# Kernel tuning notes

Hardware: AMD Instinct MI355X
Metric: run time of the kernel (lower is better)

The kernel has to match this reference:

```python
import jax, jax.numpy as jnp
import numpy as np

NEG_SLOPE = 0.01  # torch F.leaky_relu default

def _leaky(v):
    return jnp.where(v > 0, v, NEG_SLOPE * v)

def _gcn_conv(h, W, b, row, col, n_nodes):
    # PyG GCNConv with add_self_loops=True, symmetric normalization:
    # out = D^{-1/2} (A + I) D^{-1/2} (h @ W) + b,  deg includes self loop (+1)
    xw = h @ W                                            # [N, H]
    deg = jnp.zeros((n_nodes,), xw.dtype).at[col].add(1.0) + 1.0
    dis = jax.lax.rsqrt(deg)
    norm = dis[row] * dis[col]                            # [E]
    agg = jnp.zeros_like(xw).at[col].add(norm[:, None] * xw[row])
    agg = agg + xw * (1.0 / deg)[:, None]                 # self-loop term: dis_i^2 = 1/deg_i
    return agg + b

def setup_inputs() -> dict:
    key = jax.random.key(0)
    ks = jax.random.split(key, 16)
    N, E, EL = 100000, 1600000, 200000
    IN, H, EA = 256, 64, 8
    s = 0.05
    return {
        "x": jax.random.normal(ks[0], (N, IN), jnp.float32),
        "edge_index": jax.random.randint(ks[1], (2, E), 0, N, jnp.int64),
        "edge_label_index": jax.random.randint(ks[2], (2, EL), 0, N, jnp.int64),
        "edge_attr": jax.random.normal(ks[3], (EL, EA), jnp.float32),
        "W1": jax.random.normal(ks[4], (IN, 128), jnp.float32) * s,
        "b1": jnp.zeros((128,), jnp.float32),
        "W2": jax.random.normal(ks[5], (128, H), jnp.float32) * s,
        "b2": jnp.zeros((H,), jnp.float32),
        "Wg1": jax.random.normal(ks[6], (H, H), jnp.float32) * s,
        "bg1": jnp.zeros((H,), jnp.float32),
        "Wg2": jax.random.normal(ks[7], (H, H), jnp.float32) * s,
        "bg2": jnp.zeros((H,), jnp.float32),
        "Wp": jax.random.normal(ks[8], (2 * H + EA, 1), jnp.float32) * s,
        "bp": jnp.zeros((1,), jnp.float32),
    }

def reference(x, edge_index, edge_label_index, edge_attr,
              W1, b1, W2, b2, Wg1, bg1, Wg2, bg2, Wp, bp):
    n_nodes = x.shape[0]
    row, col = edge_index[0], edge_index[1]
    # preprocess MLP (dropout p=0.0 -> identity)
    h = _leaky(x @ W1 + b1)
    h = _leaky(h @ W2 + b2)
    # two GCN layers
    h = _leaky(_gcn_conv(h, Wg1, bg1, row, col, n_nodes))
    h = _leaky(_gcn_conv(h, Wg2, bg2, row, col, n_nodes))
    # edge scoring head: gather-concat-linear
    h_src = h[edge_label_index[0]]
    h_dst = h[edge_label_index[1]]
    combined = jnp.concatenate([h_src, h_dst, edge_attr], axis=1)
    out = (combined @ Wp + bp).reshape(-1)
    return (out, h)
```

## Files before the change

kernel.cpp:

```cpp
#include <hip/hip_runtime.h>
#include <hip/hip_bf16.h>

typedef __attribute__((ext_vector_type(8))) short bf16x8;
typedef __attribute__((ext_vector_type(4))) float f32x4;

#define BSHIFT 8
#define BW 256
#define NSTR 8
#define BCAP 768
#define LCAP 24
#define KEDGE 16

__device__ __forceinline__ float lk(float v) { return v > 0.f ? v : 0.01f * v; }

__device__ __forceinline__ short f2b(float v) {
  union { __hip_bfloat16 h; short s; } u;
  u.h = __float2bfloat16(v);
  return u.s;
}
__device__ __forceinline__ float loadF(const void* p, size_t i, int f32) {
  return f32 ? ((const float*)p)[i]
             : __bfloat162float(((const __hip_bfloat16*)p)[i]);
}
__device__ __forceinline__ void storeF(void* p, size_t i, int f32, float v) {
  if (f32) ((float*)p)[i] = v;
  else     ((__hip_bfloat16*)p)[i] = __float2bfloat16(v);
}
__device__ __forceinline__ int loadI(const int* p, size_t base, size_t e, int i64) {
  return i64 ? p[2 * (base + e)] : p[base + e];
}
__device__ __forceinline__ float blo(unsigned u) {
  union { unsigned u; float f; } c; c.u = u << 16; return c.f;
}
__device__ __forceinline__ float bhi(unsigned u) {
  union { unsigned u; float f; } c; c.u = u & 0xffff0000u; return c.f;
}

__global__ void detect_kernel(const unsigned short* __restrict__ x,
                              const int* __restrict__ ei, int* __restrict__ flags) {
  int t = threadIdx.x;
  unsigned short u = x[t];
  int ex = (u >> 7) & 0xFF;
  if (ex >= 0xC0) atomicOr(&flags[0], 1);
  if (t < 128 && ei[2 * t + 1] != 0) atomicOr(&flags[1], 1);
}

__global__ __launch_bounds__(64) void pack_w_kernel(const void* __restrict__ W,
                                                    __hip_bfloat16* __restrict__ P,
                                                    int N, const int* __restrict__ flags) {
  int f32 = flags[0] != 0;
  int ks = blockIdx.x, ct = blockIdx.y, KS = gridDim.x;
  int lane = threadIdx.x;
  int g = lane >> 4, m = lane & 15;
  size_t base = ((size_t)(ct * KS + ks) * 64 + (size_t)lane) * 8;
#pragma unroll
  for (int j = 0; j < 8; ++j)
    P[base + j] = __float2bfloat16(
        loadF(W, (size_t)(ks * 32 + g * 8 + j) * N + (size_t)(ct * 16 + m), f32));
}

template <int KS, int CT, int AMODE>
__global__ __launch_bounds__(256) void gemm_pipe(const void* __restrict__ A,
                                                 const __hip_bfloat16* __restrict__ Bp,
                                                 const void* __restrict__ bias,
                                                 void* __restrict__ Out, int out_bf16,
                                                 __hip_bfloat16* __restrict__ Yout,
                                                 const float* __restrict__ dinv,
                                                 int M, int N, int act,
                                                 const int* __restrict__ flags) {
  constexpr int K = KS * 32;
  constexpr int CPR = K / 8;
  constexpr int TILEB = 32 * K * 2;
  constexpr int PPR = K / 8;
  constexpr int PP = K / 64;
  __shared__ char lds[2 * TILEB];
  int f32 = AMODE ? (flags[0] != 0) : 0;
  int tid = threadIdx.x;
  int lane = tid & 63;
  int w = tid >> 6;
  int m = lane & 15, g = lane >> 4;
  int nt = (M + 31) >> 5;
  if ((int)blockIdx.x >= nt) return;

  float4 sr[2 * PP > 0 ? 2 * PP : 2];

  auto loadregs = [&](int t) {
    const float* Af = (const float*)A;
    int row0 = t << 5;
#pragma unroll
    for (int j = 0; j < PP; ++j) {
      int q = j * 256 + tid;
      int r = q / PPR;
      int pc = q - r * PPR;
      int gr = row0 + r; if (gr >= M) gr = M - 1;
      const float* src = Af + (size_t)gr * K + (size_t)pc * 8;
      sr[2 * j]     = *(const float4*)src;
      sr[2 * j + 1] = *(const float4*)(src + 4);
    }
  };
  auto cvtwrite = [&](char* buf) {
#pragma unroll
    for (int j = 0; j < PP; ++j) {
      int q = j * 256 + tid;
      int r = q / PPR;
      int pc = q - r * PPR;
      bf16x8 ov;
      ov[0] = f2b(sr[2 * j].x);     ov[1] = f2b(sr[2 * j].y);
      ov[2] = f2b(sr[2 * j].z);     ov[3] = f2b(sr[2 * j].w);
      ov[4] = f2b(sr[2 * j + 1].x); ov[5] = f2b(sr[2 * j + 1].y);
      ov[6] = f2b(sr[2 * j + 1].z); ov[7] = f2b(sr[2 * j + 1].w);
      *(bf16x8*)(buf + (size_t)r * (K * 2) + (size_t)((pc ^ (r & 7)) * 16)) = ov;
    }
  };
  auto gstage = [&](int t, char* buf) {
    int row0 = t << 5;
    constexpr int PERW = 32 * CPR / 4;
#pragma unroll
    for (int i = 0; i < PERW; i += 64) {
      int p = w * PERW + i + lane;
      int r = p / CPR;
      int pc = p - r * CPR;
      int gr = row0 + r; if (gr >= M) gr = M - 1;
      const char* src = (const char*)A + (size_t)gr * (K * 2) +
                        (size_t)((pc ^ (r & 7)) * 16);
      char* dst = buf + (size_t)(w * PERW + i) * 16;
      __builtin_amdgcn_global_load_lds(
          (const __attribute__((address_space(1))) void*)src,
          (__attribute__((address_space(3))) void*)dst, 16, 0, 0);
    }
  };

  const __hip_bfloat16* bbase = Bp + ((size_t)(w * CT) * KS * 64 + (size_t)lane) * 8;
  float bv[CT];
#pragma unroll
  for (int cc = 0; cc < CT; ++cc)
    bv[cc] = bias ? loadF(bias, (size_t)((w * CT + cc) * 16 + m), flags[0] != 0) : 0.f;

  int t0 = blockIdx.x;
  if (f32) { loadregs(t0); cvtwrite(lds); }
  else     { gstage(t0, lds); }
  __syncthreads();

  int cur = 0;
  for (int t = t0; t < nt; t += gridDim.x) {
    int tn = t + gridDim.x;
    int have = tn < nt;
    char* bufc = lds + cur * TILEB;
    char* bufn = lds + (cur ^ 1) * TILEB;
    if (have) { if (f32) loadregs(tn); else gstage(tn, bufn); }

    f32x4 accs[2][CT];
#pragma unroll
    for (int tt = 0; tt < 2; ++tt)
#pragma unroll
      for (int cc = 0; cc < CT; ++cc) accs[tt][cc] = (f32x4){0, 0, 0, 0};
#pragma unroll
    for (int ks = 0; ks < KS; ++ks) {
      bf16x8 a[2];
#pragma unroll
      for (int tt = 0; tt < 2; ++tt) {
        int r = tt * 16 + m;
        int c = ks * 4 + g;
        a[tt] = *(const bf16x8*)(bufc + (size_t)r * (K * 2) +
                                 (size_t)((c ^ (r & 7)) * 16));
      }
      const __hip_bfloat16* bb = bbase + (size_t)ks * 64 * 8;
#pragma unroll
      for (int cc = 0; cc < CT; ++cc) {
        bf16x8 b = *(const bf16x8*)(bb + (size_t)cc * KS * 64 * 8);
#pragma unroll
        for (int tt = 0; tt < 2; ++tt)
          accs[tt][cc] = __builtin_amdgcn_mfma_f32_16x16x32_bf16(a[tt], b, accs[tt][cc], 0, 0, 0);
      }
    }
    int row0 = t << 5;
#pragma unroll
    for (int tt = 0; tt < 2; ++tt) {
#pragma unroll
      for (int r = 0; r < 4; ++r) {
        int ro = row0 + tt * 16 + g * 4 + r;
        if (ro < M) {
          float di = Yout ? dinv[ro] : 0.f;
#pragma unroll
          for (int cc = 0; cc < CT; ++cc) {
            int col = (w * CT + cc) * 16 + m;
            float v = accs[tt][cc][r] + bv[cc];
            if (act) v = lk(v);
            if (Out) {
              if (out_bf16) ((__hip_bfloat16*)Out)[(size_t)ro * N + col] = __float2bfloat16(v);
              else          ((float*)Out)[(size_t)ro * N + col] = v;
            }
            if (Yout) Yout[(size_t)ro * N + col] = __float2bfloat16(v * di);
          }
        }
      }
    }
    if (have && f32) cvtwrite(bufn);
    __syncthreads();
    cur ^= 1;
  }
}

__global__ __launch_bounds__(256) void bin_kernel(const int* __restrict__ ei,
                                                  int* __restrict__ cur,
                                                  int2* __restrict__ rec,
                                                  int E, int NB,
                                                  const int* __restrict__ flags) {
  extern __shared__ int lds[];
  int* bcnt = lds;
  int* gbase = lds + NB;
  int2* bins = (int2*)(lds + 2 * NB);
  int i64 = flags[1] == 0;
  int stripe = __builtin_amdgcn_s_getreg(63508) & (NSTR - 1);
  int t = threadIdx.x;
  const int perRound = 256 * KEDGE;
  for (int base = blockIdx.x * perRound; base < E; base += gridDim.x * perRound) {
    for (int b = t; b < NB; b += 256) bcnt[b] = 0;
    __syncthreads();
#pragma unroll 1
    for (int k = 0; k < KEDGE; ++k) {
      int i = base + k * 256 + t;
      if (i < E) {
        int r, c;
        if (i64) {
          r = ((const int2*)ei)[i].x;
          c = ((const int2*)ei)[(size_t)E + i].x;
        } else {
          r = ei[i];
          c = ei[(size_t)E + i];
        }
        int b = c >> BSHIFT;
        int pos = atomicAdd(&bcnt[b], 1);
        if (pos < LCAP) {
          bins[b * LCAP + pos] = make_int2(r, c);
        } else {
          int bs = b * NSTR + stripe;
          int slot = atomicAdd(&cur[bs], 1);
          if (slot < BCAP) rec[(size_t)bs * BCAP + slot] = make_int2(r, c);
        }
      }
    }
    __syncthreads();
    for (int b = t; b < NB; b += 256) {
      int n = min(bcnt[b], LCAP);
      if (n > 0) gbase[b] = atomicAdd(&cur[b * NSTR + stripe], n);
    }
    __syncthreads();
    int lane = t & 63, w = t >> 6;
    for (int b = w; b < NB; b += 4) {
      int n = min(bcnt[b], LCAP);
      if (n == 0) continue;
      int gb = gbase[b];
      size_t sb = (size_t)(b * NSTR + stripe) * BCAP;
      if (lane < n && gb + lane < BCAP)
        rec[sb + gb + lane] = bins[b * LCAP + lane];
    }
    __syncthreads();
  }
}

__global__ __launch_bounds__(512) void bucket_scan(const int* __restrict__ cur,
                                                   int* __restrict__ bbase, int NB) {
  __shared__ int lds[512];
  int t = threadIdx.x;
  int tot = 0;
  if (t < NB)
#pragma unroll
    for (int s = 0; s < NSTR; ++s) tot += min(cur[t * NSTR + s], BCAP);
  lds[t] = tot; __syncthreads();
  for (int o = 1; o < 512; o <<= 1) {
    int a = (t >= o) ? lds[t - o] : 0; __syncthreads();
    lds[t] += a; __syncthreads();
  }
  if (t < NB) bbase[t] = lds[t] - tot;
}

__global__ __launch_bounds__(512) void place_kernel(const int2* __restrict__ rec,
                                                    const int* __restrict__ cur,
                                                    const int* __restrict__ bbase,
                                                    int* __restrict__ rowptr,
                                                    int* __restrict__ csr,
                                                    float* __restrict__ dinv, int Nn) {
  int b = blockIdx.x;
  int lo = b << BSHIFT;
  int t = threadIdx.x;
  __shared__ int cnt[BW];
  __shared__ int sc[BW];
  __shared__ int cursor[BW];
  if (t < BW) cnt[t] = 0;
  __syncthreads();
#pragma unroll 1
  for (int s = 0; s < NSTR; ++s) {
    int n = min(cur[b * NSTR + s], BCAP);
    const int2* rp = rec + (size_t)(b * NSTR + s) * BCAP;
    for (int j = t; j < n; j += 512) atomicAdd(&cnt[rp[j].y - lo], 1);
  }
  __syncthreads();
  int v = 0;
  if (t < BW) { v = cnt[t]; sc[t] = v; }
  __syncthreads();
  for (int o = 1; o < BW; o <<= 1) {
    int a = (t >= o && t < BW) ? sc[t - o] : 0;
    __syncthreads();
    if (t < BW) sc[t] += a;
    __syncthreads();
  }
  if (t < BW) {
    int base = bbase[b];
    int col = lo + t;
    if (col < Nn) {
      rowptr[col] = base + sc[t];
      dinv[col] = rsqrtf((float)v + 1.0f);
    }
    cursor[t] = base + sc[t] - v;
  }
  __syncthreads();
#pragma unroll 1
  for (int s = 0; s < NSTR; ++s) {
    int n = min(cur[b * NSTR + s], BCAP);
    const int2* rp = rec + (size_t)(b * NSTR + s) * BCAP;
    for (int j = t; j < n; j += 512) {
      int2 e = rp[j];
      int pos = atomicAdd(&cursor[e.y - lo], 1);
      csr[pos] = e.x;
    }
  }
}

__global__ __launch_bounds__(256) void gather_kernel(const __hip_bfloat16* __restrict__ y,
                                                     const int* __restrict__ csr,
                                                     const int* __restrict__ rowptr,
                                                     const float* __restrict__ dinv,
                                                     const void* __restrict__ bias,
                                                     void* __restrict__ outp, size_t obase,
                                                     int out_use_flag, int Nn,
                                                     float* __restrict__ ssrc,
                                                     float* __restrict__ sdst,
                                                     const void* __restrict__ Wp,
                                                     const int* __restrict__ flags) {
  int f32 = flags[0] != 0;
  int of32 = out_use_flag ? f32 : 0;
  int lane = threadIdx.x & 63;
  int w = (blockIdx.x * blockDim.x + threadIdx.x) >> 6;
  if (2 * w >= Nn) return;
  int half = lane >> 5;
  int hl = lane & 31;
  int hb = half << 5;
  int node = 2 * w + half;
  int alive = node < Nn;
  int nd = alive ? node : Nn - 1;
  int s = (nd == 0) ? 0 : rowptr[nd - 1];
  int e = rowptr[nd];
  if (!alive) e = s;
  const unsigned* yu = (const unsigned*)y;
  float p0a = 0, p1a = 0, p0b = 0, p1b = 0;
  float p0c = 0, p1c = 0, p0d = 0, p1d = 0;
  for (int base = s; base < e; base += 32) {
    int cnt = e - base; if (cnt > 32) cnt = 32;
    int rl = (base + hl < e) ? csr[base + hl] : 0;
    int j = 0;
    for (; j + 8 <= cnt; j += 8) {
      int r0 = __shfl(rl, hb + j + 0, 64);
      int r1 = __shfl(rl, hb + j + 1, 64);
      int r2 = __shfl(rl, hb + j + 2, 64);
      int r3 = __shfl(rl, hb + j + 3, 64);
      int r4 = __shfl(rl, hb + j + 4, 64);
      int r5 = __shfl(rl, hb + j + 5, 64);
      int r6 = __shfl(rl, hb + j + 6, 64);
      int r7 = __shfl(rl, hb + j + 7, 64);
      unsigned u0 = yu[(unsigned)r0 * 32u + hl];
      unsigned u1 = yu[(unsigned)r1 * 32u + hl];
      unsigned u2 = yu[(unsigned)r2 * 32u + hl];
      unsigned u3 = yu[(unsigned)r3 * 32u + hl];
      unsigned u4 = yu[(unsigned)r4 * 32u + hl];
      unsigned u5 = yu[(unsigned)r5 * 32u + hl];
      unsigned u6 = yu[(unsigned)r6 * 32u + hl];
      unsigned u7 = yu[(unsigned)r7 * 32u + hl];
      p0a += blo(u0); p1a += bhi(u0);
      p0b += blo(u1); p1b += bhi(u1);
      p0c += blo(u2); p1c += bhi(u2);
      p0d += blo(u3); p1d += bhi(u3);
      p0a += blo(u4); p1a += bhi(u4);
      p0b += blo(u5); p1b += bhi(u5);
      p0c += blo(u6); p1c += bhi(u6);
      p0d += blo(u7); p1d += bhi(u7);
    }
    for (; j + 4 <= cnt; j += 4) {
      int r0 = __shfl(rl, hb + j + 0, 64);
      int r1 = __shfl(rl, hb + j + 1, 64);
      int r2 = __shfl(rl, hb + j + 2, 64);
      int r3 = __shfl(rl, hb + j + 3, 64);
      unsigned u0 = yu[(unsigned)r0 * 32u + hl];
      unsigned u1 = yu[(unsigned)r1 * 32u + hl];
      unsigned u2 = yu[(unsigned)r2 * 32u + hl];
      unsigned u3 = yu[(unsigned)r3 * 32u + hl];
      p0a += blo(u0); p1a += bhi(u0);
      p0b += blo(u1); p1b += bhi(u1);
      p0c += blo(u2); p1c += bhi(u2);
      p0d += blo(u3); p1d += bhi(u3);
    }
    for (; j < cnt; ++j) {
      int r0 = __shfl(rl, hb + j, 64);
      unsigned u0 = yu[(unsigned)r0 * 32u + hl];
      p0a += blo(u0); p1a += bhi(u0);
    }
  }
  float acc0 = (p0a + p0b) + (p0c + p0d);
  float acc1 = (p1a + p1b) + (p1c + p1d);
  unsigned un = yu[(unsigned)nd * 32u + hl];
  acc0 += blo(un); acc1 += bhi(un);
  float di = dinv[nd];
  int f = hl * 2;
  float v0 = lk(di * acc0 + loadF(bias, (size_t)f, f32));
  float v1 = lk(di * acc1 + loadF(bias, (size_t)(f + 1), f32));
  if (alive) {
    if (of32) {
      *(float2*)((float*)outp + obase + (size_t)node * 64 + f) = make_float2(v0, v1);
    } else {
      union { unsigned u; unsigned short ss[2]; } pk;
      pk.ss[0] = (unsigned short)f2b(v0);
      pk.ss[1] = (unsigned short)f2b(v1);
      *(unsigned*)((__hip_bfloat16*)outp + obase + (size_t)node * 64 + f) = pk.u;
    }
  }
  if (ssrc) {
    float q1 = v0 * loadF(Wp, (size_t)f, f32) + v1 * loadF(Wp, (size_t)(f + 1), f32);
    float q2 = v0 * loadF(Wp, (size_t)(64 + f), f32) + v1 * loadF(Wp, (size_t)(65 + f), f32);
#pragma unroll
    for (int o = 16; o > 0; o >>= 1) {
      q1 += __shfl_down(q1, o, 64);
      q2 += __shfl_down(q2, o, 64);
    }
    if (hl == 0 && alive) { ssrc[node] = q1; sdst[node] = q2; }
  }
}

__global__ __launch_bounds__(256) void edge_head_kernel(void* __restrict__ dout,
                                                        const int* __restrict__ eli,
                                                        const void* __restrict__ ea,
                                                        const float* __restrict__ ssrc,
                                                        const float* __restrict__ sdst,
                                                        const void* __restrict__ Wp,
                                                        const void* __restrict__ bp,
                                                        int EL, const int* __restrict__ flags) {
  int f32 = flags[0] != 0;
  int i64 = flags[1] == 0;
  int tid = blockIdx.x * blockDim.x + threadIdx.x;
  if (tid >= EL) return;
  int s = loadI(eli, 0, (size_t)tid, i64);
  int d = loadI(eli, (size_t)EL, (size_t)tid, i64);
  float acc = ssrc[s] + sdst[d] + loadF(bp, 0, f32);
  if (f32) {
    const float* eap = (const float*)ea + (size_t)tid * 8;
    float4 u0 = *(const float4*)eap;
    float4 u1 = *(const float4*)(eap + 4);
    acc += u0.x * loadF(Wp, 128, 1) + u0.y * loadF(Wp, 129, 1) +
           u0.z * loadF(Wp, 130, 1) + u0.w * loadF(Wp, 131, 1) +
           u1.x * loadF(Wp, 132, 1) + u1.y * loadF(Wp, 133, 1) +
           u1.z * loadF(Wp, 134, 1) + u1.w * loadF(Wp, 135, 1);
  } else {
    bf16x8 u = *(const bf16x8*)((const __hip_bfloat16*)ea + (size_t)tid * 8);
#pragma unroll
    for (int j = 0; j < 8; ++j) {
      union { short s; __hip_bfloat16 h; } cv; cv.s = u[j];
      acc += __bfloat162float(cv.h) * loadF(Wp, (size_t)(128 + j), 0);
    }
  }
  storeF(dout, (size_t)tid, f32, acc);
}

extern "C" void kernel_launch(void* const* d_in, const int* in_sizes, int n_in,
                              void* d_out, int out_size, void* d_ws, size_t ws_size,
                              hipStream_t stream) {
  const void* x   = d_in[0];
  const int* ei   = (const int*)d_in[1];
  const int* eli  = (const int*)d_in[2];
  const void* ea  = d_in[3];
  const void* W1  = d_in[4];
  const void* b1  = d_in[5];
  const void* W2  = d_in[6];
  const void* b2  = d_in[7];
  const void* Wg1 = d_in[8];
  const void* bg1 = d_in[9];
  const void* Wg2 = d_in[10];
  const void* bg2 = d_in[11];
  const void* Wp  = d_in[12];
  const void* bp  = d_in[13];

  const int Nn = in_sizes[0] / 256;
  const int E  = in_sizes[1] / 2;
  const int EL = in_sizes[2] / 2;
  const int NB = (Nn + BW - 1) >> BSHIFT;

  char* ws = (char*)d_ws;
  size_t off = 0;
  auto take = [&](size_t bytes) -> char* {
    char* p = ws + off;
    off = (off + bytes + 255) & ~(size_t)255;
    return p;
  };
  int*   flags  = (int*)take(256);
  int*   cur    = (int*)take((size_t)NB * NSTR * 4);
  int*   bbase  = (int*)take((size_t)NB * 4);
  int*   rowptr = (int*)take((size_t)Nn * 4);
  float* dinv   = (float*)take((size_t)Nn * 4);
  float* ssrc   = (float*)take((size_t)Nn * 4);
  float* sdst   = (float*)take((size_t)Nn * 4);
  int*   csr    = (int*)take((size_t)E * 4);
  int2*  rec    = (int2*)take((size_t)NB * NSTR * BCAP * 8);
  __hip_bfloat16* pW1 = (__hip_bfloat16*)take(256 * 128 * 2);
  __hip_bfloat16* pW2 = (__hip_bfloat16*)take(128 * 64 * 2);
  __hip_bfloat16* pG1 = (__hip_bfloat16*)take(64 * 64 * 2);
  __hip_bfloat16* pG2 = (__hip_bfloat16*)take(64 * 64 * 2);
  char* regionA = take((size_t)Nn * 128 * 4);
  char* regionB = take((size_t)Nn * 64 * 4);
  __hip_bfloat16* h1 = (__hip_bfloat16*)regionA;
  __hip_bfloat16* y = (__hip_bfloat16*)(regionA + (size_t)Nn * 64 * 4);
  __hip_bfloat16* h2 = (__hip_bfloat16*)regionB;
  __hip_bfloat16* h3 = (__hip_bfloat16*)regionB;

  hipMemsetAsync(flags, 0, 256 + (((size_t)NB * NSTR * 4 + 255) & ~(size_t)255), stream);
  detect_kernel<<<1, 256, 0, stream>>>((const unsigned short*)x, ei, flags);

  dim3 b64(64);
  pack_w_kernel<<<dim3(8, 8), b64, 0, stream>>>(W1, pW1, 128, flags);
  pack_w_kernel<<<dim3(4, 4), b64, 0, stream>>>(W2, pW2, 64, flags);
  pack_w_kernel<<<dim3(2, 4), b64, 0, stream>>>(Wg1, pG1, 64, flags);
  pack_w_kernel<<<dim3(2, 4), b64, 0, stream>>>(Wg2, pG2, 64, flags);

  const int ldsbytes = NB * (8 + LCAP * 8);
  const int nbin = (E + 256 * KEDGE - 1) / (256 * KEDGE);
  bin_kernel<<<nbin, 256, ldsbytes, stream>>>(ei, cur, rec, E, NB, flags);
  bucket_scan<<<1, 512, 0, stream>>>(cur, bbase, NB);
  place_kernel<<<NB, 512, 0, stream>>>(rec, cur, bbase, rowptr, csr, dinv, Nn);

  const int nt = (Nn + 31) / 32;
  const int pgrid = nt < 1024 ? nt : 1024;
  gemm_pipe<8, 2, 1><<<pgrid, 256, 0, stream>>>(x, pW1, b1, h1, 1, nullptr, nullptr,
                                                Nn, 128, 1, flags);
  gemm_pipe<4, 1, 0><<<pgrid, 256, 0, stream>>>(h1, pW2, b2, h2, 1, nullptr, nullptr,
                                                Nn, 64, 1, flags);

  const int gwaves = (Nn + 1) / 2;
  const int gblocks = (gwaves + 3) / 4;
  gemm_pipe<2, 1, 0><<<pgrid, 256, 0, stream>>>(h2, pG1, nullptr, nullptr, 0, y, dinv,
                                                Nn, 64, 0, flags);
  gather_kernel<<<gblocks, 256, 0, stream>>>(y, csr, rowptr, dinv, bg1,
                                             h3, 0, 0, Nn,
                                             nullptr, nullptr, nullptr, flags);

  gemm_pipe<2, 1, 0><<<pgrid, 256, 0, stream>>>(h3, pG2, nullptr, nullptr, 0, y, dinv,
                                                Nn, 64, 0, flags);
  gather_kernel<<<gblocks, 256, 0, stream>>>(y, csr, rowptr, dinv, bg2,
                                             d_out, (size_t)EL, 1, Nn,
                                             ssrc, sdst, Wp, flags);

  edge_head_kernel<<<(EL + 255) / 256, 256, 0, stream>>>(d_out, eli, ea, ssrc, sdst,
                                                         Wp, bp, EL, flags);
}
```

Before: 402.6 us.

## Merge weight packing launches, fold bucket scan into place, use one-tile-per-block GEMMs

The four weight-pack launches are merged into one 96-block kernel, and the separate single-block bucket_scan is removed. Each place_kernel block now computes its own prefix base by reducing the counts of all preceding buckets. The persistent double-buffered GEMM is replaced by a simple one-tile-per-block kernel launched over all row tiles, trading prefetch overlap for more resident blocks and less loop bookkeeping. Together these cut kernel-launch count and serial dependencies, at the cost of redundant per-block prefix reductions and no explicit load/compute pipelining.

```diff
diff --git a/kernel.cpp b/kernel.cpp
--- a/kernel.cpp
+++ b/kernel.cpp
@@ -45,11 +45,22 @@
   if (t < 128 && ei[2 * t + 1] != 0) atomicOr(&flags[1], 1);
 }
 
-__global__ __launch_bounds__(64) void pack_w_kernel(const void* __restrict__ W,
-                                                    __hip_bfloat16* __restrict__ P,
-                                                    int N, const int* __restrict__ flags) {
+__global__ __launch_bounds__(64) void pack_all(const void* __restrict__ W1,
+                                               const void* __restrict__ W2,
+                                               const void* __restrict__ G1,
+                                               const void* __restrict__ G2,
+                                               __hip_bfloat16* __restrict__ P1,
+                                               __hip_bfloat16* __restrict__ P2,
+                                               __hip_bfloat16* __restrict__ PG1,
+                                               __hip_bfloat16* __restrict__ PG2,
+                                               const int* __restrict__ flags) {
   int f32 = flags[0] != 0;
-  int ks = blockIdx.x, ct = blockIdx.y, KS = gridDim.x;
+  int b = blockIdx.x;
+  const void* W; __hip_bfloat16* P; int KS, N, ks, ct;
+  if (b < 64)      { W = W1; P = P1;  KS = 8; N = 128; int c = b;      ks = c & 7; ct = c >> 3; }
+  else if (b < 80) { W = W2; P = P2;  KS = 4; N = 64;  int c = b - 64; ks = c & 3; ct = c >> 2; }
+  else if (b < 88) { W = G1; P = PG1; KS = 2; N = 64;  int c = b - 80; ks = c & 1; ct = c >> 1; }
+  else             { W = G2; P = PG2; KS = 2; N = 64;  int c = b - 88; ks = c & 1; ct = c >> 1; }
   int lane = threadIdx.x;
   int g = lane >> 4, m = lane & 15;
   size_t base = ((size_t)(ct * KS + ks) * 64 + (size_t)lane) * 8;
@@ -60,144 +71,120 @@
 }
 
 template <int KS, int CT, int AMODE>
-__global__ __launch_bounds__(256) void gemm_pipe(const void* __restrict__ A,
-                                                 const __hip_bfloat16* __restrict__ Bp,
-                                                 const void* __restrict__ bias,
-                                                 void* __restrict__ Out, int out_bf16,
-                                                 __hip_bfloat16* __restrict__ Yout,
-                                                 const float* __restrict__ dinv,
-                                                 int M, int N, int act,
-                                                 const int* __restrict__ flags) {
+__global__ __launch_bounds__(256) void gemm_bt(const void* __restrict__ A,
+                                               const __hip_bfloat16* __restrict__ Bp,
+                                               const void* __restrict__ bias,
+                                               void* __restrict__ Out, int out_bf16,
+                                               __hip_bfloat16* __restrict__ Yout,
+                                               const float* __restrict__ dinv,
+                                               int M, int N, int act,
+                                               const int* __restrict__ flags) {
   constexpr int K = KS * 32;
   constexpr int CPR = K / 8;
-  constexpr int TILEB = 32 * K * 2;
-  constexpr int PPR = K / 8;
-  constexpr int PP = K / 64;
-  __shared__ char lds[2 * TILEB];
+  __shared__ char tile[32 * K * 2];
   int f32 = AMODE ? (flags[0] != 0) : 0;
   int tid = threadIdx.x;
   int lane = tid & 63;
   int w = tid >> 6;
   int m = lane & 15, g = lane >> 4;
-  int nt = (M + 31) >> 5;
-  if ((int)blockIdx.x >= nt) return;
-
-  float4 sr[2 * PP > 0 ? 2 * PP : 2];
-
-  auto loadregs = [&](int t) {
-    const float* Af = (const float*)A;
-    int row0 = t << 5;
-#pragma unroll
-    for (int j = 0; j < PP; ++j) {
-      int q = j * 256 + tid;
-      int r = q / PPR;
-      int pc = q - r * PPR;
-      int gr = row0 + r; if (gr >= M) gr = M - 1;
-      const float* src = Af + (size_t)gr * K + (size_t)pc * 8;
-      sr[2 * j]     = *(const float4*)src;
-      sr[2 * j + 1] = *(const float4*)(src + 4);
-    }
-  };
-  auto cvtwrite = [&](char* buf) {
-#pragma unroll
-    for (int j = 0; j < PP; ++j) {
-      int q = j * 256 + tid;
-      int r = q / PPR;
-      int pc = q - r * PPR;
-      bf16x8 ov;
-      ov[0] = f2b(sr[2 * j].x);     ov[1] = f2b(sr[2 * j].y);
-      ov[2] = f2b(sr[2 * j].z);     ov[3] = f2b(sr[2 * j].w);
-      ov[4] = f2b(sr[2 * j + 1].x); ov[5] = f2b(sr[2 * j + 1].y);
-      ov[6] = f2b(sr[2 * j + 1].z); ov[7] = f2b(sr[2 * j + 1].w);
-      *(bf16x8*)(buf + (size_t)r * (K * 2) + (size_t)((pc ^ (r & 7)) * 16)) = ov;
-    }
-  };
-  auto gstage = [&](int t, char* buf) {
-    int row0 = t << 5;
+  int row0 = blockIdx.x << 5;
+
+  bool done = false;
+  if constexpr (AMODE) {
+    if (f32) {
+      constexpr int PP = K / 64;
+      float4 sr[2 * PP];
+#pragma unroll
+      for (int j = 0; j < PP; ++j) {
+        int q = j * 256 + tid;
+        int r = q / CPR, pc = q - r * CPR;
+        int gr = row0 + r; if (gr >= M) gr = M - 1;
+        const float* src = (const float*)A + (size_t)gr * K + (size_t)pc * 8;
+        sr[2 * j]     = *(const float4*)src;
+        sr[2 * j + 1] = *(const float4*)(src + 4);
+      }
+#pragma unroll
+      for (int j = 0; j < PP; ++j) {
+        int q = j * 256 + tid;
+        int r = q / CPR, pc = q - r * CPR;
+        bf16x8 ov;
+        ov[0] = f2b(sr[2 * j].x);     ov[1] = f2b(sr[2 * j].y);
+        ov[2] = f2b(sr[2 * j].z);     ov[3] = f2b(sr[2 * j].w);
+        ov[4] = f2b(sr[2 * j + 1].x); ov[5] = f2b(sr[2 * j + 1].y);
+        ov[6] = f2b(sr[2 * j + 1].z); ov[7] = f2b(sr[2 * j + 1].w);
+        *(bf16x8*)(tile + (size_t)r * (K * 2) + (size_t)((pc ^ (r & 7)) * 16)) = ov;
+      }
+      done = true;
+    }
+  }
+  if (!done) {
     constexpr int PERW = 32 * CPR / 4;
 #pragma unroll
     for (int i = 0; i < PERW; i += 64) {
       int p = w * PERW + i + lane;
-      int r = p / CPR;
-      int pc = p - r * CPR;
+      int r = p / CPR, pc = p - r * CPR;
       int gr = row0 + r; if (gr >= M) gr = M - 1;
       const char* src = (const char*)A + (size_t)gr * (K * 2) +
                         (size_t)((pc ^ (r & 7)) * 16);
-      char* dst = buf + (size_t)(w * PERW + i) * 16;
+      char* dst = tile + (size_t)(w * PERW + i) * 16;
       __builtin_amdgcn_global_load_lds(
           (const __attribute__((address_space(1))) void*)src,
           (__attribute__((address_space(3))) void*)dst, 16, 0, 0);
     }
-  };
+  }
+  __syncthreads();
 
   const __hip_bfloat16* bbase = Bp + ((size_t)(w * CT) * KS * 64 + (size_t)lane) * 8;
+  f32x4 accs[2][CT];
+#pragma unroll
+  for (int tt = 0; tt < 2; ++tt)
+#pragma unroll
+    for (int cc = 0; cc < CT; ++cc) accs[tt][cc] = (f32x4){0, 0, 0, 0};
+
+#pragma unroll
+  for (int ks = 0; ks < KS; ++ks) {
+    bf16x8 a[2];
+#pragma unroll
+    for (int tt = 0; tt < 2; ++tt) {
+      int r = tt * 16 + m;
+      int c = ks * 4 + g;
+      a[tt] = *(const bf16x8*)(tile + (size_t)r * (K * 2) +
+                               (size_t)((c ^ (r & 7)) * 16));
+    }
+    const __hip_bfloat16* bb = bbase + (size_t)ks * 64 * 8;
+#pragma unroll
+    for (int cc = 0; cc < CT; ++cc) {
+      bf16x8 b = *(const bf16x8*)(bb + (size_t)cc * KS * 64 * 8);
+#pragma unroll
+      for (int tt = 0; tt < 2; ++tt)
+        accs[tt][cc] = __builtin_amdgcn_mfma_f32_16x16x32_bf16(a[tt], b, accs[tt][cc], 0, 0, 0);
+    }
+  }
+
   float bv[CT];
 #pragma unroll
   for (int cc = 0; cc < CT; ++cc)
     bv[cc] = bias ? loadF(bias, (size_t)((w * CT + cc) * 16 + m), flags[0] != 0) : 0.f;
-
-  int t0 = blockIdx.x;
-  if (f32) { loadregs(t0); cvtwrite(lds); }
-  else     { gstage(t0, lds); }
-  __syncthreads();
-
-  int cur = 0;
-  for (int t = t0; t < nt; t += gridDim.x) {
-    int tn = t + gridDim.x;
-    int have = tn < nt;
-    char* bufc = lds + cur * TILEB;
-    char* bufn = lds + (cur ^ 1) * TILEB;
-    if (have) { if (f32) loadregs(tn); else gstage(tn, bufn); }
-
-    f32x4 accs[2][CT];
-#pragma unroll
-    for (int tt = 0; tt < 2; ++tt)
-#pragma unroll
-      for (int cc = 0; cc < CT; ++cc) accs[tt][cc] = (f32x4){0, 0, 0, 0};
-#pragma unroll
-    for (int ks = 0; ks < KS; ++ks) {
-      bf16x8 a[2];
-#pragma unroll
-      for (int tt = 0; tt < 2; ++tt) {
-        int r = tt * 16 + m;
-        int c = ks * 4 + g;
-        a[tt] = *(const bf16x8*)(bufc + (size_t)r * (K * 2) +
-                                 (size_t)((c ^ (r & 7)) * 16));
-      }
-      const __hip_bfloat16* bb = bbase + (size_t)ks * 64 * 8;
-#pragma unroll
-      for (int cc = 0; cc < CT; ++cc) {
-        bf16x8 b = *(const bf16x8*)(bb + (size_t)cc * KS * 64 * 8);
-#pragma unroll
-        for (int tt = 0; tt < 2; ++tt)
-          accs[tt][cc] = __builtin_amdgcn_mfma_f32_16x16x32_bf16(a[tt], b, accs[tt][cc], 0, 0, 0);
-      }
-    }
-    int row0 = t << 5;
-#pragma unroll
-    for (int tt = 0; tt < 2; ++tt) {
-#pragma unroll
-      for (int r = 0; r < 4; ++r) {
-        int ro = row0 + tt * 16 + g * 4 + r;
-        if (ro < M) {
-          float di = Yout ? dinv[ro] : 0.f;
-#pragma unroll
-          for (int cc = 0; cc < CT; ++cc) {
-            int col = (w * CT + cc) * 16 + m;
-            float v = accs[tt][cc][r] + bv[cc];
-            if (act) v = lk(v);
-            if (Out) {
-              if (out_bf16) ((__hip_bfloat16*)Out)[(size_t)ro * N + col] = __float2bfloat16(v);
-              else          ((float*)Out)[(size_t)ro * N + col] = v;
-            }
-            if (Yout) Yout[(size_t)ro * N + col] = __float2bfloat16(v * di);
+#pragma unroll
+  for (int tt = 0; tt < 2; ++tt) {
+#pragma unroll
+    for (int r = 0; r < 4; ++r) {
+      int ro = row0 + tt * 16 + g * 4 + r;
+      if (ro < M) {
+        float di = Yout ? dinv[ro] : 0.f;
+#pragma unroll
+        for (int cc = 0; cc < CT; ++cc) {
+          int col = (w * CT + cc) * 16 + m;
+          float v = accs[tt][cc][r] + bv[cc];
+          if (act) v = lk(v);
+          if (Out) {
+            if (out_bf16) ((__hip_bfloat16*)Out)[(size_t)ro * N + col] = __float2bfloat16(v);
+            else          ((float*)Out)[(size_t)ro * N + col] = v;
           }
+          if (Yout) Yout[(size_t)ro * N + col] = __float2bfloat16(v * di);
         }
       }
     }
-    if (have && f32) cvtwrite(bufn);
-    __syncthreads();
-    cur ^= 1;
   }
 }
 
@@ -259,25 +246,8 @@
   }
 }
 
-__global__ __launch_bounds__(512) void bucket_scan(const int* __restrict__ cur,
-                                                   int* __restrict__ bbase, int NB) {
-  __shared__ int lds[512];
-  int t = threadIdx.x;
-  int tot = 0;
-  if (t < NB)
-#pragma unroll
-    for (int s = 0; s < NSTR; ++s) tot += min(cur[t * NSTR + s], BCAP);
-  lds[t] = tot; __syncthreads();
-  for (int o = 1; o < 512; o <<= 1) {
-    int a = (t >= o) ? lds[t - o] : 0; __syncthreads();
-    lds[t] += a; __syncthreads();
-  }
-  if (t < NB) bbase[t] = lds[t] - tot;
-}
-
 __global__ __launch_bounds__(512) void place_kernel(const int2* __restrict__ rec,
                                                     const int* __restrict__ cur,
-                                                    const int* __restrict__ bbase,
                                                     int* __restrict__ rowptr,
                                                     int* __restrict__ csr,
                                                     float* __restrict__ dinv, int Nn) {
@@ -287,8 +257,17 @@
   __shared__ int cnt[BW];
   __shared__ int sc[BW];
   __shared__ int cursor[BW];
+  __shared__ int red[512];
+  int part = 0;
+  for (int i = t; i < b * NSTR; i += 512) part += min(cur[i], BCAP);
+  red[t] = part;
   if (t < BW) cnt[t] = 0;
   __syncthreads();
+  for (int o = 256; o > 0; o >>= 1) {
+    if (t < o) red[t] += red[t + o];
+    __syncthreads();
+  }
+  int base = red[0];
 #pragma unroll 1
   for (int s = 0; s < NSTR; ++s) {
     int n = min(cur[b * NSTR + s], BCAP);
@@ -306,7 +285,6 @@
     __syncthreads();
   }
   if (t < BW) {
-    int base = bbase[b];
     int col = lo + t;
     if (col < Nn) {
       rowptr[col] = base + sc[t];
@@ -501,7 +479,6 @@
   };
   int*   flags  = (int*)take(256);
   int*   cur    = (int*)take((size_t)NB * NSTR * 4);
-  int*   bbase  = (int*)take((size_t)NB * 4);
   int*   rowptr = (int*)take((size_t)Nn * 4);
   float* dinv   = (float*)take((size_t)Nn * 4);
   float* ssrc   = (float*)take((size_t)Nn * 4);
@@ -522,34 +499,28 @@
   hipMemsetAsync(flags, 0, 256 + (((size_t)NB * NSTR * 4 + 255) & ~(size_t)255), stream);
   detect_kernel<<<1, 256, 0, stream>>>((const unsigned short*)x, ei, flags);
 
-  dim3 b64(64);
-  pack_w_kernel<<<dim3(8, 8), b64, 0, stream>>>(W1, pW1, 128, flags);
-  pack_w_kernel<<<dim3(4, 4), b64, 0, stream>>>(W2, pW2, 64, flags);
-  pack_w_kernel<<<dim3(2, 4), b64, 0, stream>>>(Wg1, pG1, 64, flags);
-  pack_w_kernel<<<dim3(2, 4), b64, 0, stream>>>(Wg2, pG2, 64, flags);
+  pack_all<<<96, 64, 0, stream>>>(W1, W2, Wg1, Wg2, pW1, pW2, pG1, pG2, flags);
 
   const int ldsbytes = NB * (8 + LCAP * 8);
   const int nbin = (E + 256 * KEDGE - 1) / (256 * KEDGE);
   bin_kernel<<<nbin, 256, ldsbytes, stream>>>(ei, cur, rec, E, NB, flags);
-  bucket_scan<<<1, 512, 0, stream>>>(cur, bbase, NB);
-  place_kernel<<<NB, 512, 0, stream>>>(rec, cur, bbase, rowptr, csr, dinv, Nn);
-
-  const int nt = (Nn + 31) / 32;
-  const int pgrid = nt < 1024 ? nt : 1024;
-  gemm_pipe<8, 2, 1><<<pgrid, 256, 0, stream>>>(x, pW1, b1, h1, 1, nullptr, nullptr,
+  place_kernel<<<NB, 512, 0, stream>>>(rec, cur, rowptr, csr, dinv, Nn);
+
+  const int tblocks = (Nn + 31) / 32;
+  gemm_bt<8, 2, 1><<<tblocks, 256, 0, stream>>>(x, pW1, b1, h1, 1, nullptr, nullptr,
                                                 Nn, 128, 1, flags);
-  gemm_pipe<4, 1, 0><<<pgrid, 256, 0, stream>>>(h1, pW2, b2, h2, 1, nullptr, nullptr,
+  gemm_bt<4, 1, 0><<<tblocks, 256, 0, stream>>>(h1, pW2, b2, h2, 1, nullptr, nullptr,
                                                 Nn, 64, 1, flags);
 
   const int gwaves = (Nn + 1) / 2;
   const int gblocks = (gwaves + 3) / 4;
-  gemm_pipe<2, 1, 0><<<pgrid, 256, 0, stream>>>(h2, pG1, nullptr, nullptr, 0, y, dinv,
+  gemm_bt<2, 1, 0><<<tblocks, 256, 0, stream>>>(h2, pG1, nullptr, nullptr, 0, y, dinv,
                                                 Nn, 64, 0, flags);
   gather_kernel<<<gblocks, 256, 0, stream>>>(y, csr, rowptr, dinv, bg1,
                                              h3, 0, 0, Nn,
                                              nullptr, nullptr, nullptr, flags);
 
-  gemm_pipe<2, 1, 0><<<pgrid, 256, 0, stream>>>(h3, pG2, nullptr, nullptr, 0, y, dinv,
+  gemm_bt<2, 1, 0><<<tblocks, 256, 0, stream>>>(h3, pG2, nullptr, nullptr, 0, y, dinv,
                                                 Nn, 64, 0, flags);
   gather_kernel<<<gblocks, 256, 0, stream>>>(y, csr, rowptr, dinv, bg2,
                                              d_out, (size_t)EL, 1, Nn,
```

New measurement: 372.7 us. 7.4% less time.
